# Performance work log

Hardware: AMD Instinct MI355X
Metric: run time of the kernel (lower is better)

## Reference

```python
import jax, jax.numpy as jnp
import numpy as np

ALPHA = 0.025
BETA = 0.00025
V_TH = 1.0
EXP_TAU = 50.0          # tau_v / dt
T_NOW = 10.0            # current simulation step counter self.t
REFRAC_STEPS = 2        # refractory_period / dt
INV_TAU_V = float(np.exp(-1.0 / 50.0))   # exp(-dt/tau_v)
INV_TAU_I = float(np.exp(-1.0))          # exp(-dt/tau_i)
INV_TAU_V_PAIR = INV_TAU_V               # tau_v_pair defaults to tau_v
INV_TAU_I_PAIR = INV_TAU_I               # tau_i_pair defaults to tau_i

B, N = 32, 4096


def setup_inputs() -> dict:
    key = jax.random.key(0)
    ks = jax.random.split(key, 8)
    return {
        "inp": jax.random.normal(ks[0], (B, N), jnp.float32),
        "W_rec": jax.random.uniform(ks[1], (N, N), jnp.float32),  # nonneg dense adjacency weights
        "mem_pot": jax.random.normal(ks[2], (B, N), jnp.float32),
        "mem_cur": jax.random.normal(ks[3], (B, N), jnp.float32),
        "mem_pot_paired": jax.random.normal(ks[4], (B, N), jnp.float32),
        "mem_cur_paired": jax.random.normal(ks[5], (B, N), jnp.float32),
        "st": jnp.zeros((N,), jnp.float32),
        "refrac_neurons": jax.random.randint(ks[6], (B, N), 0, 3, jnp.int32),
    }


def reference(inp, W_rec, mem_pot, mem_cur, mem_pot_paired, mem_cur_paired, st, refrac_neurons):
    sign_mask = W_rec > 0  # torch: sign(W_rec) > 0 (weights are nonneg)

    # decrement refractory counters
    refrac = jnp.where(refrac_neurons > 0, refrac_neurons - 1, refrac_neurons)

    # threshold (ceil+clamp -> {0,1} spikes)
    S = jnp.clip(jnp.ceil(mem_pot - V_TH), 0.0, 1.0)                     # (B,N)
    S_paired = jnp.clip(jnp.ceil(mem_pot_paired - V_TH - ALPHA), 0.0, 1.0)

    # ---- plasticity weight update ----
    sp_max = S_paired.max(axis=0)            # (N,)
    st_new = jnp.where(S > 0, T_NOW, st)     # broadcasts (N,) -> (B,N), as in torch
    max_st = st_new.max(axis=0)              # (N,)
    # meshgrid(a,b) with ij indexing: |a-b|[i,j] = |max_st[i]-max_st[j]|
    diff = jnp.abs(max_st[:, None] - max_st[None, :])                    # (N,N)
    update_mask = (sp_max[:, None] > 0) & sign_mask                      # (N,N)
    updated = W_rec + BETA - jnp.where(update_mask,
                                       ALPHA * jnp.exp(diff / EXP_TAU),
                                       0.0)
    updated = jnp.clip(updated, 0.0, 1.0)
    W_new = jnp.where(sign_mask, updated, W_rec)

    # ---- integrate ----
    active = refrac == 0
    mem_cur_n = jnp.where(active, inp + S @ W_new + mem_cur, mem_cur)
    mem_cur_p_n = jnp.where(active, S @ W_new.T + mem_cur_paired, mem_cur_paired)
    mem_pot_n = jnp.where(active, mem_cur_n + mem_pot, mem_pot)
    mem_pot_p_n = jnp.where(active, mem_cur_p_n + mem_pot_paired, mem_pot_paired)

    # leak
    mem_pot_n = mem_pot_n * INV_TAU_V
    mem_cur_n = mem_cur_n * INV_TAU_I
    mem_pot_p_n = mem_pot_p_n * INV_TAU_V_PAIR
    mem_cur_p_n = mem_cur_p_n * INV_TAU_I_PAIR

    # reset spiked neurons
    mem_pot_n = jnp.where(S > 0, 0.0, mem_pot_n)
    mem_pot_p_n = jnp.where(S_paired > 0, 0.0, mem_pot_p_n)
    refrac_new = jnp.where(S > 0, REFRAC_STEPS, refrac)

    return S, mem_pot_n, W_new, mem_cur_n, mem_pot_p_n, mem_cur_p_n, refrac_new
```

## Files before the change

kernel.cpp:

```cpp
#include <hip/hip_runtime.h>
#include <cstdint>
#include <cstddef>

constexpr int N = 4096;
constexpr int B = 32;
constexpr int BN = B * N;
constexpr size_t NN = (size_t)N * N;

constexpr int TI = 128;
constexpr int TJ = 128;
constexpr int NIT = N / TI;
constexpr int NJT = N / TJ;
constexpr int ISUB = 64;
constexpr int LDT = TJ + 8;

constexpr float ALPHA = 0.025f;
constexpr float BETA = 0.00025f;
constexpr float T_NOW = 10.0f;
constexpr float INV_EXP_TAU = 0.02f;
constexpr float INV_TAU_V = 0.98019867f;
constexpr float INV_TAU_I = 0.36787944f;

typedef __attribute__((ext_vector_type(8))) short short8;
typedef __attribute__((ext_vector_type(4))) float f32x4;

__device__ inline unsigned short f2bf(float f) {
  uint32_t u = __float_as_uint(f);
  u += 0x7FFFu + ((u >> 16) & 1u);
  return (unsigned short)(u >> 16);
}

__device__ inline float wupd(float w, float mrow, float frow, float mcol) {
  float d = fabsf(mrow - mcol);
  float u = w + BETA - frow * __expf(d * INV_EXP_TAU);
  u = fminf(fmaxf(u, 0.0f), 1.0f);
  return (w > 0.0f) ? u : w;
}

__global__ __launch_bounds__(256) void pass_a(
    const float* __restrict__ mem_pot, const float* __restrict__ mem_pot_p,
    const float* __restrict__ st, float* __restrict__ S_out,
    unsigned short* __restrict__ S_bf,
    uint32_t* __restrict__ maskS, uint32_t* __restrict__ maskSP,
    float* __restrict__ max_st, float* __restrict__ rowfac) {
  int j = blockIdx.x * blockDim.x + threadIdx.x;
  if (j >= N) return;
  float stj = st[j];
  uint32_t ms = 0u, msp = 0u;
  float maxv = -3.0e38f;
  #pragma unroll
  for (int b = 0; b < B; ++b) {
    float p = mem_pot[b * N + j];
    float pp = mem_pot_p[b * N + j];
    bool s = (p - 1.0f) > 0.0f;
    bool sp = ((pp - 1.0f) - ALPHA) > 0.0f;
    S_out[b * N + j] = s ? 1.0f : 0.0f;
    S_bf[b * N + j] = s ? 0x3F80u : 0u;
    ms |= (uint32_t)s << b;
    msp |= (uint32_t)sp << b;
    maxv = fmaxf(maxv, s ? T_NOW : stj);
  }
  maskS[j] = ms;
  maskSP[j] = msp;
  max_st[j] = maxv;
  rowfac[j] = msp ? ALPHA : 0.0f;
}

__global__ __launch_bounds__(256, 3) void pass_fused(
    const float* __restrict__ W, const unsigned short* __restrict__ S_bf,
    const float* __restrict__ max_st, const float* __restrict__ rowfac,
    float* __restrict__ Wout, float* __restrict__ partSW,
    float* __restrict__ partSWT) {
  __shared__ __align__(16) unsigned short tile[ISUB * LDT];
  __shared__ float mstI[TI];
  __shared__ float facI[TI];
  __shared__ float mstJ[TJ];

  int tid = threadIdx.x;
  int wv = tid >> 6;
  int lane = tid & 63;
  int quad = lane >> 4;
  int nl = lane & 15;
  int jt = blockIdx.x;
  int it = blockIdx.y;
  int i0 = it * TI;
  int j0 = jt * TJ;

  uint32_t* tileU32 = (uint32_t*)tile;

  int row8 = tid >> 5;
  int c4 = tid & 31;

  float4 pf[8];
  {
    const float* base = W + (size_t)(i0 + row8) * N + j0 + c4 * 4;
    #pragma unroll
    for (int p = 0; p < 8; ++p)
      pf[p] = *(const float4*)(base + (size_t)(p * 8) * N);
  }

  if (tid < TI) {
    mstI[tid] = max_st[i0 + tid];
    facI[tid] = rowfac[i0 + tid];
  } else {
    mstJ[tid - TI] = max_st[j0 + (tid - TI)];
  }

  short8 aG0[4], aG1[4], aJ0[4], aJ1[4];
  if (wv < 3) {
    #pragma unroll
    for (int c = 0; c < 4; ++c) {
      aG0[c] = *(const short8*)(S_bf + (size_t)nl * N + i0 + c * 32 + quad * 8);
      aG1[c] = *(const short8*)(S_bf + (size_t)(nl + 16) * N + i0 + c * 32 + quad * 8);
    }
  } else {
    #pragma unroll
    for (int c = 0; c < 4; ++c) {
      aJ0[c] = *(const short8*)(S_bf + (size_t)nl * N + j0 + c * 32 + quad * 8);
      aJ1[c] = *(const short8*)(S_bf + (size_t)(nl + 16) * N + j0 + c * 32 + quad * 8);
    }
  }
  __syncthreads();

  f32x4 accG0[3], accG1[3];
  #pragma unroll
  for (int t = 0; t < 3; ++t) {
    accG0[t] = (f32x4){0.f, 0.f, 0.f, 0.f};
    accG1[t] = (f32x4){0.f, 0.f, 0.f, 0.f};
  }

  #pragma unroll
  for (int isub = 0; isub < TI / ISUB; ++isub) {
    float4 mj = *(const float4*)(mstJ + c4 * 4);
    #pragma unroll
    for (int p = 0; p < 8; ++p) {
      int r = p * 8 + row8;
      int ig = i0 + isub * ISUB + r;
      float mi = mstI[isub * ISUB + r];
      float fi = facI[isub * ISUB + r];
      f32x4 u;
      u[0] = wupd(pf[p].x, mi, fi, mj.x);
      u[1] = wupd(pf[p].y, mi, fi, mj.y);
      u[2] = wupd(pf[p].z, mi, fi, mj.z);
      u[3] = wupd(pf[p].w, mi, fi, mj.w);
      __builtin_nontemporal_store(u, (f32x4*)(Wout + (size_t)ig * N + j0 + c4 * 4));
      uint32_t d0 = (uint32_t)f2bf(u[0]) | ((uint32_t)f2bf(u[1]) << 16);
      uint32_t d1 = (uint32_t)f2bf(u[2]) | ((uint32_t)f2bf(u[3]) << 16);
      uint2 dd; dd.x = d0; dd.y = d1;
      *(uint2*)&tileU32[r * (LDT / 2) + c4 * 2] = dd;
    }
    if (isub + 1 < TI / ISUB) {
      const float* base =
          W + (size_t)(i0 + (isub + 1) * ISUB + row8) * N + j0 + c4 * 4;
      #pragma unroll
      for (int p = 0; p < 8; ++p)
        pf[p] = *(const float4*)(base + (size_t)(p * 8) * N);
    }
    __syncthreads();

    if (wv < 3) {
      #pragma unroll
      for (int t = 0; t < 3; ++t) {
        int js = wv + 3 * t;
        if (js < 8) {
          #pragma unroll
          for (int kstep = 0; kstep < 2; ++kstep) {
            int kl = kstep * 32 + quad * 8;
            int c = isub * 2 + kstep;
            short8 b;
            #pragma unroll
            for (int e = 0; e < 8; ++e)
              b[e] = (short)tile[(kl + e) * LDT + js * 16 + nl];
            accG0[t] = __builtin_amdgcn_mfma_f32_16x16x32_bf16(aG0[c], b, accG0[t], 0, 0, 0);
            accG1[t] = __builtin_amdgcn_mfma_f32_16x16x32_bf16(aG1[c], b, accG1[t], 0, 0, 0);
          }
        }
      }
    } else {
      #pragma unroll
      for (int g = 0; g < 4; ++g) {
        int il = g * 16 + nl;
        f32x4 g0 = {0.f, 0.f, 0.f, 0.f}, g1 = {0.f, 0.f, 0.f, 0.f};
        #pragma unroll
        for (int kstep = 0; kstep < 4; ++kstep) {
          int kl = kstep * 32 + quad * 8;
          short8 bfr = *(const short8*)&tile[il * LDT + kl];
          g0 = __builtin_amdgcn_mfma_f32_16x16x32_bf16(aJ0[kstep], bfr, g0, 0, 0, 0);
          g1 = __builtin_amdgcn_mfma_f32_16x16x32_bf16(aJ1[kstep], bfr, g1, 0, 0, 0);
        }
        int iglob = i0 + isub * ISUB + il;
        size_t basew = (size_t)jt * BN + iglob;
        #pragma unroll
        for (int r = 0; r < 4; ++r) {
          partSWT[basew + (size_t)(quad * 4 + r) * N] = g0[r];
          partSWT[basew + (size_t)(16 + quad * 4 + r) * N] = g1[r];
        }
      }
    }
    if (isub + 1 < TI / ISUB) __syncthreads();
  }

  if (wv < 3) {
    size_t baseit = (size_t)it * BN;
    #pragma unroll
    for (int t = 0; t < 3; ++t) {
      int js = wv + 3 * t;
      if (js < 8) {
        int jg = j0 + js * 16 + nl;
        #pragma unroll
        for (int r = 0; r < 4; ++r) {
          partSW[baseit + (size_t)(quad * 4 + r) * N + jg] = accG0[t][r];
          partSW[baseit + (size_t)(16 + quad * 4 + r) * N + jg] = accG1[t][r];
        }
      }
    }
  }
}

__global__ __launch_bounds__(256) void pass_d(
    const float* __restrict__ inp, const float* __restrict__ mem_pot,
    const float* __restrict__ mem_cur, const float* __restrict__ mem_pot_p,
    const float* __restrict__ mem_cur_p, const int* __restrict__ refrac_in,
    const uint32_t* __restrict__ maskS, const uint32_t* __restrict__ maskSP,
    const float* __restrict__ partSW, const float* __restrict__ partSWT,
    float* __restrict__ pot_out, float* __restrict__ cur_out,
    float* __restrict__ potp_out, float* __restrict__ curp_out,
    float* __restrict__ refrac_out) {
  int e = blockIdx.x * 256 + threadIdx.x;
  int b = e >> 12;
  int j = e & (N - 1);

  float SW = 0.0f, SWT = 0.0f;
  #pragma unroll
  for (int c = 0; c < NIT; ++c) SW += partSW[(size_t)c * BN + e];
  #pragma unroll
  for (int c = 0; c < NJT; ++c) SWT += partSWT[(size_t)c * BN + e];

  int r = refrac_in[e];
  int rd = (r > 0) ? (r - 1) : r;
  bool active = (rd == 0);
  bool s = (maskS[j] >> b) & 1u;
  bool sp = (maskSP[j] >> b) & 1u;
  float cur = mem_cur[e], pot = mem_pot[e];
  float curp = mem_cur_p[e], potp = mem_pot_p[e];

  float cur_n = active ? (inp[e] + SW + cur) : cur;
  float curp_n = active ? (SWT + curp) : curp;
  float pot_n = active ? (cur_n + pot) : pot;
  float potp_n = active ? (curp_n + potp) : potp;

  pot_n *= INV_TAU_V;
  cur_n *= INV_TAU_I;
  potp_n *= INV_TAU_V;
  curp_n *= INV_TAU_I;

  if (s) pot_n = 0.0f;
  if (sp) potp_n = 0.0f;
  int rn = s ? 2 : rd;

  pot_out[e] = pot_n;
  cur_out[e] = cur_n;
  potp_out[e] = potp_n;
  curp_out[e] = curp_n;
  refrac_out[e] = (float)rn;
}

extern "C" void kernel_launch(void* const* d_in, const int* in_sizes, int n_in,
                              void* d_out, int out_size, void* d_ws, size_t ws_size,
                              hipStream_t stream) {
  const float* inp = (const float*)d_in[0];
  const float* W = (const float*)d_in[1];
  const float* mem_pot = (const float*)d_in[2];
  const float* mem_cur = (const float*)d_in[3];
  const float* mem_pot_p = (const float*)d_in[4];
  const float* mem_cur_p = (const float*)d_in[5];
  const float* st = (const float*)d_in[6];
  const int* refrac = (const int*)d_in[7];

  float* out = (float*)d_out;
  float* S_out = out;
  float* pot_out = out + BN;
  float* W_out = out + 2 * (size_t)BN;
  float* cur_out = W_out + NN;
  float* potp_out = cur_out + BN;
  float* curp_out = potp_out + BN;
  float* refrac_out = curp_out + BN;

  uint32_t* maskS = (uint32_t*)d_ws;
  uint32_t* maskSP = maskS + N;
  float* max_st = (float*)(maskSP + N);
  float* rowfac = max_st + N;
  unsigned short* S_bf = (unsigned short*)(rowfac + N);
  float* partSW = (float*)(S_bf + BN);
  float* partSWT = partSW + (size_t)NIT * BN;

  pass_a<<<N / 256, 256, 0, stream>>>(mem_pot, mem_pot_p, st, S_out, S_bf,
                                      maskS, maskSP, max_st, rowfac);
  pass_fused<<<dim3(NJT, NIT), 256, 0, stream>>>(W, S_bf, max_st, rowfac,
                                                 W_out, partSW, partSWT);
  pass_d<<<BN / 256, 256, 0, stream>>>(inp, mem_pot, mem_cur, mem_pot_p,
                                       mem_cur_p, refrac, maskS, maskSP,
                                       partSW, partSWT, pot_out, cur_out,
                                       potp_out, curp_out, refrac_out);
}
```

Before: 161.8 us.

## Split fused weight-update pass into separate GEMM block roles with swizzled LDS

Replaces the single fused tile kernel, where one block updated W and fed both GEMMs, with a kernel that has two block roles. One role updates W, writes W_out, and computes S@W^T over 512-column chunks. The other role recomputes the update to compute S@W over 256-row chunks. Partial-sum buffers shrink (16 and 8 slices instead of 32 each), and an XOR-swizzled LDS layout is used for the transposed GEMM. In exchange, W is read from memory twice and the plasticity update is computed twice.

```diff
diff --git a/kernel.cpp b/kernel.cpp
--- a/kernel.cpp
+++ b/kernel.cpp
@@ -7,12 +7,11 @@
 constexpr int BN = B * N;
 constexpr size_t NN = (size_t)N * N;
 
-constexpr int TI = 128;
-constexpr int TJ = 128;
-constexpr int NIT = N / TI;
-constexpr int NJT = N / TJ;
-constexpr int ISUB = 64;
-constexpr int LDT = TJ + 8;
+constexpr int ABLK = 256;
+constexpr int BBLK = 512;
+constexpr int NPSWT = 8;
+constexpr int NPSW = 16;
+constexpr int LDTB = 136;
 
 constexpr float ALPHA = 0.025f;
 constexpr float BETA = 0.00025f;
@@ -66,152 +65,194 @@
   rowfac[j] = msp ? ALPHA : 0.0f;
 }
 
-__global__ __launch_bounds__(256, 3) void pass_fused(
+__global__ __launch_bounds__(256, 3) void pass_gemms(
     const float* __restrict__ W, const unsigned short* __restrict__ S_bf,
     const float* __restrict__ max_st, const float* __restrict__ rowfac,
     float* __restrict__ Wout, float* __restrict__ partSW,
     float* __restrict__ partSWT) {
-  __shared__ __align__(16) unsigned short tile[ISUB * LDT];
-  __shared__ float mstI[TI];
-  __shared__ float facI[TI];
-  __shared__ float mstJ[TJ];
+  __shared__ __align__(16) char smem[33792];
 
   int tid = threadIdx.x;
   int wv = tid >> 6;
   int lane = tid & 63;
   int quad = lane >> 4;
   int nl = lane & 15;
-  int jt = blockIdx.x;
-  int it = blockIdx.y;
-  int i0 = it * TI;
-  int j0 = jt * TJ;
-
-  uint32_t* tileU32 = (uint32_t*)tile;
-
   int row8 = tid >> 5;
   int c4 = tid & 31;
 
-  float4 pf[8];
-  {
-    const float* base = W + (size_t)(i0 + row8) * N + j0 + c4 * 4;
+  if (blockIdx.x < ABLK) {
+    int it = blockIdx.x & 31;
+    int jc = blockIdx.x >> 5;
+    int i0 = it * 128;
+    float* mstIA = (float*)(smem + 32768);
+    float* facIA = mstIA + 128;
+
+    if (tid < 128) {
+      mstIA[tid] = max_st[i0 + tid];
+      facIA[tid] = rowfac[i0 + tid];
+    }
+
+    f32x4 acc[2][2];
     #pragma unroll
-    for (int p = 0; p < 8; ++p)
-      pf[p] = *(const float4*)(base + (size_t)(p * 8) * N);
-  }
-
-  if (tid < TI) {
-    mstI[tid] = max_st[i0 + tid];
-    facI[tid] = rowfac[i0 + tid];
+    for (int a = 0; a < 2; ++a)
+      #pragma unroll
+      for (int h = 0; h < 2; ++h) acc[a][h] = (f32x4){0.f, 0.f, 0.f, 0.f};
+
+    __syncthreads();
+
+    #pragma unroll 1
+    for (int jsub = 0; jsub < 4; ++jsub) {
+      int jb = jc * 512 + jsub * 128;
+      float4 pf[16];
+      const float* wb = W + (size_t)(i0 + row8) * N + jb + c4 * 4;
+      #pragma unroll
+      for (int p = 0; p < 16; ++p)
+        pf[p] = *(const float4*)(wb + (size_t)(p * 8) * N);
+      short8 aA0[4], aA1[4];
+      #pragma unroll
+      for (int ks = 0; ks < 4; ++ks) {
+        int kg = jb + ks * 32 + quad * 8;
+        aA0[ks] = *(const short8*)(S_bf + (size_t)nl * N + kg);
+        aA1[ks] = *(const short8*)(S_bf + (size_t)(nl + 16) * N + kg);
+      }
+      float4 mj4 = *(const float4*)(max_st + jb + c4 * 4);
+
+      #pragma unroll
+      for (int p = 0; p < 16; ++p) {
+        int r = p * 8 + row8;
+        float mi = mstIA[r];
+        float fi = facIA[r];
+        f32x4 u;
+        u[0] = wupd(pf[p].x, mi, fi, mj4.x);
+        u[1] = wupd(pf[p].y, mi, fi, mj4.y);
+        u[2] = wupd(pf[p].z, mi, fi, mj4.z);
+        u[3] = wupd(pf[p].w, mi, fi, mj4.w);
+        __builtin_nontemporal_store(
+            u, (f32x4*)(Wout + (size_t)(i0 + r) * N + jb + c4 * 4));
+        uint32_t d0 = (uint32_t)f2bf(u[0]) | ((uint32_t)f2bf(u[1]) << 16);
+        uint32_t d1 = (uint32_t)f2bf(u[2]) | ((uint32_t)f2bf(u[3]) << 16);
+        uint2 dd; dd.x = d0; dd.y = d1;
+        *(uint2*)(smem + r * 256 + ((((c4 >> 1) ^ (r & 7))) << 4) +
+                  ((c4 & 1) << 3)) = dd;
+      }
+      __syncthreads();
+
+      #pragma unroll
+      for (int ks = 0; ks < 4; ++ks) {
+        #pragma unroll
+        for (int nt = 0; nt < 2; ++nt) {
+          int rr = wv * 32 + nt * 16 + nl;
+          short8 bfr = *(const short8*)(
+              smem + rr * 256 + ((((ks * 4 + quad) ^ (rr & 7))) << 4));
+          acc[nt][0] =
+              __builtin_amdgcn_mfma_f32_16x16x32_bf16(aA0[ks], bfr, acc[nt][0], 0, 0, 0);
+          acc[nt][1] =
+              __builtin_amdgcn_mfma_f32_16x16x32_bf16(aA1[ks], bfr, acc[nt][1], 0, 0, 0);
+        }
+      }
+      if (jsub < 3) __syncthreads();
+    }
+
+    size_t baseA = (size_t)jc * BN;
+    #pragma unroll
+    for (int nt = 0; nt < 2; ++nt) {
+      int ig = i0 + wv * 32 + nt * 16 + nl;
+      #pragma unroll
+      for (int r = 0; r < 4; ++r) {
+        partSWT[baseA + (size_t)(quad * 4 + r) * N + ig] = acc[nt][0][r];
+        partSWT[baseA + (size_t)(16 + quad * 4 + r) * N + ig] = acc[nt][1][r];
+      }
+    }
   } else {
-    mstJ[tid - TI] = max_st[j0 + (tid - TI)];
-  }
-
-  short8 aG0[4], aG1[4], aJ0[4], aJ1[4];
-  if (wv < 3) {
+    int idx = blockIdx.x - ABLK;
+    int jt = idx & 31;
+    int ic = idx >> 5;
+    int j0 = jt * 128;
+    int ibase = ic * 256;
+    unsigned short* tileB = (unsigned short*)smem;
+    float* mstIB = (float*)(smem + 17408);
+    float* facIB = mstIB + 256;
+    float* mstJB = facIB + 256;
+
+    mstIB[tid] = max_st[ibase + tid];
+    facIB[tid] = rowfac[ibase + tid];
+    if (tid < 128) mstJB[tid] = max_st[j0 + tid];
+
+    float4 pf[8];
+    {
+      const float* wb = W + (size_t)(ibase + row8) * N + j0 + c4 * 4;
+      #pragma unroll
+      for (int p = 0; p < 8; ++p)
+        pf[p] = *(const float4*)(wb + (size_t)(p * 8) * N);
+    }
+
+    f32x4 accB[2][2];
     #pragma unroll
-    for (int c = 0; c < 4; ++c) {
-      aG0[c] = *(const short8*)(S_bf + (size_t)nl * N + i0 + c * 32 + quad * 8);
-      aG1[c] = *(const short8*)(S_bf + (size_t)(nl + 16) * N + i0 + c * 32 + quad * 8);
-    }
-  } else {
+    for (int a = 0; a < 2; ++a)
+      #pragma unroll
+      for (int h = 0; h < 2; ++h) accB[a][h] = (f32x4){0.f, 0.f, 0.f, 0.f};
+
+    __syncthreads();
+
+    #pragma unroll 1
+    for (int isub = 0; isub < 4; ++isub) {
+      short8 aB0[2], aB1[2];
+      #pragma unroll
+      for (int ks = 0; ks < 2; ++ks) {
+        int kg = ibase + isub * 64 + ks * 32 + quad * 8;
+        aB0[ks] = *(const short8*)(S_bf + (size_t)nl * N + kg);
+        aB1[ks] = *(const short8*)(S_bf + (size_t)(nl + 16) * N + kg);
+      }
+      float4 mjB = *(const float4*)(mstJB + c4 * 4);
+      #pragma unroll
+      for (int p = 0; p < 8; ++p) {
+        int r = p * 8 + row8;
+        float mi = mstIB[isub * 64 + r];
+        float fi = facIB[isub * 64 + r];
+        float ux = wupd(pf[p].x, mi, fi, mjB.x);
+        float uy = wupd(pf[p].y, mi, fi, mjB.y);
+        float uz = wupd(pf[p].z, mi, fi, mjB.z);
+        float uw = wupd(pf[p].w, mi, fi, mjB.w);
+        uint32_t d0 = (uint32_t)f2bf(ux) | ((uint32_t)f2bf(uy) << 16);
+        uint32_t d1 = (uint32_t)f2bf(uz) | ((uint32_t)f2bf(uw) << 16);
+        uint2 dd; dd.x = d0; dd.y = d1;
+        *(uint2*)((char*)tileB + r * (LDTB * 2) + c4 * 8) = dd;
+      }
+      if (isub + 1 < 4) {
+        const float* wb =
+            W + (size_t)(ibase + (isub + 1) * 64 + row8) * N + j0 + c4 * 4;
+        #pragma unroll
+        for (int p = 0; p < 8; ++p)
+          pf[p] = *(const float4*)(wb + (size_t)(p * 8) * N);
+      }
+      __syncthreads();
+
+      #pragma unroll
+      for (int ks = 0; ks < 2; ++ks) {
+        #pragma unroll
+        for (int t = 0; t < 2; ++t) {
+          int js = wv * 2 + t;
+          short8 b;
+          #pragma unroll
+          for (int e = 0; e < 8; ++e)
+            b[e] = (short)tileB[(ks * 32 + quad * 8 + e) * LDTB + js * 16 + nl];
+          accB[t][0] =
+              __builtin_amdgcn_mfma_f32_16x16x32_bf16(aB0[ks], b, accB[t][0], 0, 0, 0);
+          accB[t][1] =
+              __builtin_amdgcn_mfma_f32_16x16x32_bf16(aB1[ks], b, accB[t][1], 0, 0, 0);
+        }
+      }
+      if (isub + 1 < 4) __syncthreads();
+    }
+
+    size_t baseB = (size_t)ic * BN;
     #pragma unroll
-    for (int c = 0; c < 4; ++c) {
-      aJ0[c] = *(const short8*)(S_bf + (size_t)nl * N + j0 + c * 32 + quad * 8);
-      aJ1[c] = *(const short8*)(S_bf + (size_t)(nl + 16) * N + j0 + c * 32 + quad * 8);
-    }
-  }
-  __syncthreads();
-
-  f32x4 accG0[3], accG1[3];
-  #pragma unroll
-  for (int t = 0; t < 3; ++t) {
-    accG0[t] = (f32x4){0.f, 0.f, 0.f, 0.f};
-    accG1[t] = (f32x4){0.f, 0.f, 0.f, 0.f};
-  }
-
-  #pragma unroll
-  for (int isub = 0; isub < TI / ISUB; ++isub) {
-    float4 mj = *(const float4*)(mstJ + c4 * 4);
-    #pragma unroll
-    for (int p = 0; p < 8; ++p) {
-      int r = p * 8 + row8;
-      int ig = i0 + isub * ISUB + r;
-      float mi = mstI[isub * ISUB + r];
-      float fi = facI[isub * ISUB + r];
-      f32x4 u;
-      u[0] = wupd(pf[p].x, mi, fi, mj.x);
-      u[1] = wupd(pf[p].y, mi, fi, mj.y);
-      u[2] = wupd(pf[p].z, mi, fi, mj.z);
-      u[3] = wupd(pf[p].w, mi, fi, mj.w);
-      __builtin_nontemporal_store(u, (f32x4*)(Wout + (size_t)ig * N + j0 + c4 * 4));
-      uint32_t d0 = (uint32_t)f2bf(u[0]) | ((uint32_t)f2bf(u[1]) << 16);
-      uint32_t d1 = (uint32_t)f2bf(u[2]) | ((uint32_t)f2bf(u[3]) << 16);
-      uint2 dd; dd.x = d0; dd.y = d1;
-      *(uint2*)&tileU32[r * (LDT / 2) + c4 * 2] = dd;
-    }
-    if (isub + 1 < TI / ISUB) {
-      const float* base =
-          W + (size_t)(i0 + (isub + 1) * ISUB + row8) * N + j0 + c4 * 4;
-      #pragma unroll
-      for (int p = 0; p < 8; ++p)
-        pf[p] = *(const float4*)(base + (size_t)(p * 8) * N);
-    }
-    __syncthreads();
-
-    if (wv < 3) {
-      #pragma unroll
-      for (int t = 0; t < 3; ++t) {
-        int js = wv + 3 * t;
-        if (js < 8) {
-          #pragma unroll
-          for (int kstep = 0; kstep < 2; ++kstep) {
-            int kl = kstep * 32 + quad * 8;
-            int c = isub * 2 + kstep;
-            short8 b;
-            #pragma unroll
-            for (int e = 0; e < 8; ++e)
-              b[e] = (short)tile[(kl + e) * LDT + js * 16 + nl];
-            accG0[t] = __builtin_amdgcn_mfma_f32_16x16x32_bf16(aG0[c], b, accG0[t], 0, 0, 0);
-            accG1[t] = __builtin_amdgcn_mfma_f32_16x16x32_bf16(aG1[c], b, accG1[t], 0, 0, 0);
-          }
-        }
-      }
-    } else {
-      #pragma unroll
-      for (int g = 0; g < 4; ++g) {
-        int il = g * 16 + nl;
-        f32x4 g0 = {0.f, 0.f, 0.f, 0.f}, g1 = {0.f, 0.f, 0.f, 0.f};
-        #pragma unroll
-        for (int kstep = 0; kstep < 4; ++kstep) {
-          int kl = kstep * 32 + quad * 8;
-          short8 bfr = *(const short8*)&tile[il * LDT + kl];
-          g0 = __builtin_amdgcn_mfma_f32_16x16x32_bf16(aJ0[kstep], bfr, g0, 0, 0, 0);
-          g1 = __builtin_amdgcn_mfma_f32_16x16x32_bf16(aJ1[kstep], bfr, g1, 0, 0, 0);
-        }
-        int iglob = i0 + isub * ISUB + il;
-        size_t basew = (size_t)jt * BN + iglob;
-        #pragma unroll
-        for (int r = 0; r < 4; ++r) {
-          partSWT[basew + (size_t)(quad * 4 + r) * N] = g0[r];
-          partSWT[basew + (size_t)(16 + quad * 4 + r) * N] = g1[r];
-        }
-      }
-    }
-    if (isub + 1 < TI / ISUB) __syncthreads();
-  }
-
-  if (wv < 3) {
-    size_t baseit = (size_t)it * BN;
-    #pragma unroll
-    for (int t = 0; t < 3; ++t) {
-      int js = wv + 3 * t;
-      if (js < 8) {
-        int jg = j0 + js * 16 + nl;
-        #pragma unroll
-        for (int r = 0; r < 4; ++r) {
-          partSW[baseit + (size_t)(quad * 4 + r) * N + jg] = accG0[t][r];
-          partSW[baseit + (size_t)(16 + quad * 4 + r) * N + jg] = accG1[t][r];
-        }
+    for (int t = 0; t < 2; ++t) {
+      int jg = j0 + (wv * 2 + t) * 16 + nl;
+      #pragma unroll
+      for (int r = 0; r < 4; ++r) {
+        partSW[baseB + (size_t)(quad * 4 + r) * N + jg] = accB[t][0][r];
+        partSW[baseB + (size_t)(16 + quad * 4 + r) * N + jg] = accB[t][1][r];
       }
     }
   }
@@ -232,9 +273,9 @@
 
   float SW = 0.0f, SWT = 0.0f;
   #pragma unroll
-  for (int c = 0; c < NIT; ++c) SW += partSW[(size_t)c * BN + e];
+  for (int c = 0; c < NPSW; ++c) SW += partSW[(size_t)c * BN + e];
   #pragma unroll
-  for (int c = 0; c < NJT; ++c) SWT += partSWT[(size_t)c * BN + e];
+  for (int c = 0; c < NPSWT; ++c) SWT += partSWT[(size_t)c * BN + e];
 
   int r = refrac_in[e];
   int rd = (r > 0) ? (r - 1) : r;
@@ -292,12 +333,12 @@
   float* rowfac = max_st + N;
   unsigned short* S_bf = (unsigned short*)(rowfac + N);
   float* partSW = (float*)(S_bf + BN);
-  float* partSWT = partSW + (size_t)NIT * BN;
+  float* partSWT = partSW + (size_t)NPSW * BN;
 
   pass_a<<<N / 256, 256, 0, stream>>>(mem_pot, mem_pot_p, st, S_out, S_bf,
                                       maskS, maskSP, max_st, rowfac);
-  pass_fused<<<dim3(NJT, NIT), 256, 0, stream>>>(W, S_bf, max_st, rowfac,
-                                                 W_out, partSW, partSWT);
+  pass_gemms<<<ABLK + BBLK, 256, 0, stream>>>(W, S_bf, max_st, rowfac,
+                                              W_out, partSW, partSWT);
   pass_d<<<BN / 256, 256, 0, stream>>>(inp, mem_pot, mem_cur, mem_pot_p,
                                        mem_cur_p, refrac, maskS, maskSP,
                                        partSW, partSWT, pot_out, cur_out,
```

Result: faster. 155.0 us (-4.2%).
